# Optimization experiments

Hardware: AMD Instinct MI355X
Metric: run time of the kernel (lower is better)

The kernel has to match this reference:

```python
import jax, jax.numpy as jnp
import numpy as np

BS, IN_F, OUT_F = 1024, 128, 100000
M, S, ALPHA = 0.35, 30.0, 0.5


def _l2norm(x):
    # F.normalize: x / max(||x||, eps)
    n = jnp.sqrt(jnp.sum(x * x, axis=-1, keepdims=True))
    return x / jnp.maximum(n, 1e-12)


def setup_inputs() -> dict:
    key = jax.random.key(0)
    k1, k2, k3 = jax.random.split(key, 3)
    return {
        "input": jax.random.normal(k1, (BS, IN_F), dtype=jnp.float32),
        "label": jax.random.randint(k2, (BS,), 0, OUT_F, dtype=jnp.int64),
        "weight": jax.random.normal(k3, (OUT_F, IN_F), dtype=jnp.float32),
    }


def reference(input, label, weight):
    wn = _l2norm(weight)                      # [nc, d]
    fn = _l2norm(input)                       # [bs, d]
    logits = jnp.einsum('bd,cd->bc', fn, wn)  # [bs, nc] cosine sims
    bs = fn.shape[0]
    rows = jnp.arange(bs)

    pos = jnp.take_along_axis(logits, label[:, None], axis=1)[:, 0] * S  # [bs]
    # negatives: all classes except the label (replaces masked_select + view)
    neg = (logits * S).at[rows, label].set(-jnp.inf)
    lse_neg = jax.nn.logsumexp(neg, axis=1)   # [bs]

    # loss = mean(log(1 + exp(m + lse_neg - pos)))
    loss = jnp.mean(jax.nn.softplus(M + lse_neg - pos))

    # weight.data update: per-class mean of normalized features for classes
    # present in the batch (the torch loop is exactly a segment-mean; note
    # weight_update aliases weight.data so the final blend is a no-op and the
    # result is simply: present rows <- class mean, other rows unchanged).
    sums = jax.ops.segment_sum(fn, label, num_segments=OUT_F)                # [nc, d]
    counts = jax.ops.segment_sum(jnp.ones((bs,), fn.dtype), label, num_segments=OUT_F)
    present = counts > 0
    class_mean = sums / jnp.maximum(counts, 1.0)[:, None]
    new_weight = jnp.where(present[:, None], class_mean, weight)

    return loss, new_weight
```

## Files before the change

kernel.cpp:

```cpp
#include <hip/hip_runtime.h>

#define BS 1024
#define D 128
#define NC 100000
#define NCP 100096
#define NT64 1564
#define PHASES 256
#define S_SCALE 30.0f
#define MARGIN 0.35f
#define S2LOG2E 43.2808512f

typedef __attribute__((ext_vector_type(8))) short bf16x8;
typedef __attribute__((ext_vector_type(4))) float f32x4;

__device__ __forceinline__ unsigned short f2bf(float f) {
    union { float f; unsigned u; } x; x.f = f;
    unsigned u = x.u;
    u += 0x7FFFu + ((u >> 16) & 1u);
    return (unsigned short)(u >> 16);
}

__device__ __forceinline__ void gld_lds16(const void* g, void* l) {
    auto gp = (const __attribute__((address_space(1))) unsigned int*)(g);
    auto lp = (__attribute__((address_space(3))) unsigned int*)(l);
    __builtin_amdgcn_global_load_lds(gp, lp, 16, 0, 0);
}


__global__ void prep_fn(const float* __restrict__ inp, const int* __restrict__ label,
                        const float* __restrict__ wt,
                        float* __restrict__ fn_f32, unsigned short* __restrict__ fn_fr,
                        float* __restrict__ counts, float* __restrict__ pos) {
    int row = blockIdx.x * 4 + (threadIdx.x >> 6);
    int lane = threadIdx.x & 63;
    float2 v = *(const float2*)(inp + row * D + lane * 2);
    float s = v.x * v.x + v.y * v.y;
    #pragma unroll
    for (int m = 1; m < 64; m <<= 1) s += __shfl_xor(s, m);
    float inv = 1.0f / fmaxf(sqrtf(s), 1e-12f);
    float a = v.x * inv, b = v.y * inv;
    *(float2*)(fn_f32 + row * D + lane * 2) = make_float2(a, b);
    unsigned pack = (unsigned)f2bf(a) | ((unsigned)f2bf(b) << 16);
    ((unsigned*)fn_fr)[(row >> 4) * 1024 + (lane >> 2) * 64 + ((row & 15) << 2) + (lane & 3)] = pack;

    int c = label[row];
    float2 wv = *(const float2*)(wt + c * D + lane * 2);
    float sw_ = wv.x * wv.x + wv.y * wv.y;
    float dt  = wv.x * a + wv.y * b;
    #pragma unroll
    for (int m = 1; m < 64; m <<= 1) { sw_ += __shfl_xor(sw_, m); dt += __shfl_xor(dt, m); }
    if (lane == 0) {
        float invw = 1.0f / fmaxf(sqrtf(sw_), 1e-12f);
        pos[row] = S_SCALE * dt * invw;
        atomicAdd(counts + c, 1.0f);
    }
}

__global__ void prep_wn(const float* __restrict__ wt, const float* __restrict__ counts,
                        unsigned short* __restrict__ wn_fr, float* __restrict__ outw) {
    int wv = threadIdx.x >> 6, lane = threadIdx.x & 63;
    int row = blockIdx.x * 4 + wv;
    unsigned* dst = (unsigned*)wn_fr + (row >> 4) * 1024 + (lane >> 2) * 64 +
                    ((row & 15) << 2) + (lane & 3);
    if (row < NC) {
        float2 v = *(const float2*)(wt + row * D + lane * 2);
        float s = v.x * v.x + v.y * v.y;
        #pragma unroll
        for (int m = 1; m < 64; m <<= 1) s += __shfl_xor(s, m);
        float inv = 1.0f / fmaxf(sqrtf(s), 1e-12f);
        *dst = (unsigned)f2bf(v.x * inv) | ((unsigned)f2bf(v.y * inv) << 16);
        float cnt = counts[row];
        float2 o = (cnt > 0.0f) ? make_float2(0.0f, 0.0f) : v;
        *(float2*)(outw + row * D + lane * 2) = o;
    } else {
        *dst = 0u;
    }
}

__global__ __launch_bounds__(1024, 4) void main_gemm(
    const unsigned short* __restrict__ fnfr, const unsigned short* __restrict__ wnfr,
    float* __restrict__ sumexp) {
    __shared__ __align__(16) short Ws[2][8192];
    int tid = threadIdx.x;
    int lane = tid & 63, w = tid >> 6;
    int half = blockIdx.y;
    int rb0 = half * 32 + w * 2;

    bf16x8 bf[2][4];
    {
        const char* gB = (const char*)fnfr + (size_t)rb0 * 4096 + lane * 16;
        #pragma unroll
        for (int cg = 0; cg < 2; cg++)
            #pragma unroll
            for (int ks = 0; ks < 4; ks++)
                bf[cg][ks] = *(const bf16x8*)(gB + cg * 4096 + ks * 1024);
    }
    #pragma unroll
    for (int cg = 0; cg < 2; cg++)
        #pragma unroll
        for (int ks = 0; ks < 4; ks++)
            asm volatile("" : "+v"(bf[cg][ks]));

    float sums[2] = {0.0f, 0.0f};

    int t0 = blockIdx.x;
    {
        const char* g = (const char*)wnfr + (size_t)t0 * 16384 + w * 1024 + lane * 16;
        gld_lds16(g, (char*)Ws[0] + w * 1024);
    }
    __syncthreads();

    int cur = 0;
    for (int t = t0; t < NT64; t += PHASES) {
        int nxt = t + PHASES;
        if (nxt < NT64) {
            const char* g = (const char*)wnfr + (size_t)nxt * 16384 + w * 1024 + lane * 16;
            gld_lds16(g, (char*)Ws[cur ^ 1] + w * 1024);
        }

        f32x4 acc[4][2];
        #pragma unroll
        for (int ag = 0; ag < 4; ag++)
            #pragma unroll
            for (int cg = 0; cg < 2; cg++)
                acc[ag][cg] = (f32x4){0.0f, 0.0f, 0.0f, 0.0f};

        const char* W = (const char*)Ws[cur];
        #pragma unroll
        for (int ks = 0; ks < 4; ks++) {
            bf16x8 a[4];
            #pragma unroll
            for (int ag = 0; ag < 4; ag++)
                a[ag] = *(const bf16x8*)(W + ag * 4096 + ks * 1024 + lane * 16);
            #pragma unroll
            for (int ag = 0; ag < 4; ag++)
                #pragma unroll
                for (int cg = 0; cg < 2; cg++)
                    acc[ag][cg] = __builtin_amdgcn_mfma_f32_16x16x32_bf16(
                        a[ag], bf[cg][ks], acc[ag][cg], 0, 0, 0);
        }

        #pragma unroll
        for (int ag = 0; ag < 4; ag++)
            #pragma unroll
            for (int cg = 0; cg < 2; cg++)
                #pragma unroll
                for (int r = 0; r < 4; r++)
                    sums[cg] += __builtin_amdgcn_exp2f(
                        fmaf(acc[ag][cg][r], S2LOG2E, -S2LOG2E));

        __syncthreads();
        cur ^= 1;
    }

    #pragma unroll
    for (int cg = 0; cg < 2; cg++) {
        float s = sums[cg];
        s += __shfl_xor(s, 16);
        s += __shfl_xor(s, 32);
        if (lane < 16)
            atomicAdd(sumexp + half * 512 + w * 32 + cg * 16 + lane, s);
    }
}

__global__ void loss_k(const float* __restrict__ sumexp, const float* __restrict__ pos,
                       float* __restrict__ out) {
    __shared__ float red[256];
    int t = threadIdx.x;
    float acc = 0.0f;
    #pragma unroll
    for (int i = 0; i < 4; i++) {
        int r = t + i * 256;
        float p = pos[r];
        float sneg = fmaxf(sumexp[r] - __expf(p - 30.0f), 1e-38f);
        float lse = 30.0f + logf(sneg);
        float z = MARGIN + lse - p;
        acc += fmaxf(z, 0.0f) + log1pf(__expf(-fabsf(z)));
    }
    red[t] = acc;
    __syncthreads();
    for (int s = 128; s > 0; s >>= 1) {
        if (t < s) red[t] += red[t + s];
        __syncthreads();
    }
    if (t == 0) out[0] = red[0] * (1.0f / 1024.0f);
}

__global__ void addmean_k(const float* __restrict__ fn_f32, const int* __restrict__ label,
                          const float* __restrict__ counts, float* __restrict__ outw) {
    int b = blockIdx.x, t = threadIdx.x;
    int c = label[b];
    float cnt = counts[c];
    atomicAdd(outw + c * D + t, fn_f32[b * D + t] / cnt);
}

extern "C" void kernel_launch(void* const* d_in, const int* in_sizes, int n_in,
                              void* d_out, int out_size, void* d_ws, size_t ws_size,
                              hipStream_t stream) {
    (void)in_sizes; (void)n_in; (void)out_size; (void)ws_size;
    const float* inp   = (const float*)d_in[0];
    const int*   label = (const int*)d_in[1];
    const float* wt    = (const float*)d_in[2];
    float* out = (float*)d_out;

    char* w = (char*)d_ws;
    float*          fn_f32 = (float*)(w);
    unsigned short* fn_fr  = (unsigned short*)(w + 524288);
    unsigned short* wn_fr  = (unsigned short*)(w + 786432);
    float*          sumexp = (float*)(w + 26411008);
    float*          counts = (float*)(w + 26415104);
    float*          pos    = (float*)(w + 26815104);

    hipMemsetAsync(w + 26411008, 0, 404096, stream);

    prep_fn<<<BS / 4, 256, 0, stream>>>(inp, label, wt, fn_f32, fn_fr, counts, pos);
    prep_wn<<<NCP / 4, 256, 0, stream>>>(wt, counts, wn_fr, out + 1);
    main_gemm<<<dim3(PHASES, 2), 1024, 0, stream>>>(fn_fr, wn_fr, sumexp);
    addmean_k<<<BS, D, 0, stream>>>(fn_f32, label, counts, out + 1);
    loss_k<<<1, 256, 0, stream>>>(sumexp, pos, out);
}
```

Measured before the change: 160.3 us.

## Fuse weight normalization into GEMM and merge tail kernels

Removes the separate prep_wn pass by having the GEMM load fp32 weight rows directly, normalize and convert them to bf16 in registers, and write them into the LDS double buffer. The half-0 blocks also write the untouched weight rows to the output. The addmean and loss kernels are merged into one launch. This drops a 25MB bf16 intermediate write and read plus two launches. In exchange, each of the two y-halves now reads the fp32 weights (twice the bytes of bf16) and adds normalization ALU work inside the GEMM loop.

```diff
diff --git a/kernel.cpp b/kernel.cpp
--- a/kernel.cpp
+++ b/kernel.cpp
@@ -20,12 +20,6 @@
     return (unsigned short)(u >> 16);
 }
 
-__device__ __forceinline__ void gld_lds16(const void* g, void* l) {
-    auto gp = (const __attribute__((address_space(1))) unsigned int*)(g);
-    auto lp = (__attribute__((address_space(3))) unsigned int*)(l);
-    __builtin_amdgcn_global_load_lds(gp, lp, 16, 0, 0);
-}
-
 
 __global__ void prep_fn(const float* __restrict__ inp, const int* __restrict__ label,
                         const float* __restrict__ wt,
@@ -56,39 +50,52 @@
     }
 }
 
-__global__ void prep_wn(const float* __restrict__ wt, const float* __restrict__ counts,
-                        unsigned short* __restrict__ wn_fr, float* __restrict__ outw) {
-    int wv = threadIdx.x >> 6, lane = threadIdx.x & 63;
-    int row = blockIdx.x * 4 + wv;
-    unsigned* dst = (unsigned*)wn_fr + (row >> 4) * 1024 + (lane >> 2) * 64 +
-                    ((row & 15) << 2) + (lane & 3);
-    if (row < NC) {
-        float2 v = *(const float2*)(wt + row * D + lane * 2);
-        float s = v.x * v.x + v.y * v.y;
-        #pragma unroll
-        for (int m = 1; m < 64; m <<= 1) s += __shfl_xor(s, m);
-        float inv = 1.0f / fmaxf(sqrtf(s), 1e-12f);
-        *dst = (unsigned)f2bf(v.x * inv) | ((unsigned)f2bf(v.y * inv) << 16);
-        float cnt = counts[row];
-        float2 o = (cnt > 0.0f) ? make_float2(0.0f, 0.0f) : v;
-        *(float2*)(outw + row * D + lane * 2) = o;
-    } else {
-        *dst = 0u;
-    }
-}
+#define LOADV()  do {                                                         \
+    if (rg < NC) {                                                            \
+        const float* p_ = wt + (size_t)rg * 128 + 2 * g16;                    \
+        v0 = *(const float2*)(p_);      v1 = *(const float2*)(p_ + 32);       \
+        v2 = *(const float2*)(p_ + 64); v3 = *(const float2*)(p_ + 96);       \
+    } else { v0 = v1 = v2 = v3 = make_float2(0.f, 0.f); }                     \
+} while (0)
+
+#define COMMIT(buf) do {                                                      \
+    float ss = v0.x*v0.x + v0.y*v0.y + v1.x*v1.x + v1.y*v1.y                  \
+             + v2.x*v2.x + v2.y*v2.y + v3.x*v3.x + v3.y*v3.y;                 \
+    ss += __shfl_xor(ss, 1); ss += __shfl_xor(ss, 2);                         \
+    ss += __shfl_xor(ss, 4); ss += __shfl_xor(ss, 8);                         \
+    float inv = 1.0f / fmaxf(sqrtf(ss), 1e-12f);                              \
+    unsigned* Wu_ = (unsigned*)(buf);                                         \
+    int base_ = (rloc >> 4) * 1024 + (g16 >> 2) * 64 + (rloc & 15) * 4 + (g16 & 3); \
+    Wu_[base_]       = (unsigned)f2bf(v0.x*inv) | ((unsigned)f2bf(v0.y*inv) << 16); \
+    Wu_[base_ + 256] = (unsigned)f2bf(v1.x*inv) | ((unsigned)f2bf(v1.y*inv) << 16); \
+    Wu_[base_ + 512] = (unsigned)f2bf(v2.x*inv) | ((unsigned)f2bf(v2.y*inv) << 16); \
+    Wu_[base_ + 768] = (unsigned)f2bf(v3.x*inv) | ((unsigned)f2bf(v3.y*inv) << 16); \
+    if (writeout && rg < NC) {                                                \
+        float cnt_ = counts[rg];                                              \
+        float* op_ = outw + (size_t)rg * 128 + 2 * g16;                       \
+        float2 z_ = make_float2(0.f, 0.f);                                    \
+        *(float2*)(op_)      = (cnt_ > 0.f) ? z_ : v0;                        \
+        *(float2*)(op_ + 32) = (cnt_ > 0.f) ? z_ : v1;                        \
+        *(float2*)(op_ + 64) = (cnt_ > 0.f) ? z_ : v2;                        \
+        *(float2*)(op_ + 96) = (cnt_ > 0.f) ? z_ : v3;                        \
+    }                                                                         \
+} while (0)
 
 __global__ __launch_bounds__(1024, 4) void main_gemm(
-    const unsigned short* __restrict__ fnfr, const unsigned short* __restrict__ wnfr,
-    float* __restrict__ sumexp) {
+    const unsigned short* __restrict__ fnfr, const float* __restrict__ wt,
+    const float* __restrict__ counts, float* __restrict__ sumexp,
+    float* __restrict__ outw) {
     __shared__ __align__(16) short Ws[2][8192];
-    int tid = threadIdx.x;
-    int lane = tid & 63, w = tid >> 6;
-    int half = blockIdx.y;
-    int rb0 = half * 32 + w * 2;
+    const int tid = threadIdx.x;
+    const int lane = tid & 63, w = tid >> 6;
+    const int g16 = tid & 15;
+    const int rloc = tid >> 4;
+    const int half = blockIdx.y;
+    const bool writeout = (half == 0);
 
     bf16x8 bf[2][4];
     {
-        const char* gB = (const char*)fnfr + (size_t)rb0 * 4096 + lane * 16;
+        const char* gB = (const char*)fnfr + (size_t)(half * 32 + w * 2) * 4096 + lane * 16;
         #pragma unroll
         for (int cg = 0; cg < 2; cg++)
             #pragma unroll
@@ -102,21 +109,17 @@
             asm volatile("" : "+v"(bf[cg][ks]));
 
     float sums[2] = {0.0f, 0.0f};
-
-    int t0 = blockIdx.x;
-    {
-        const char* g = (const char*)wnfr + (size_t)t0 * 16384 + w * 1024 + lane * 16;
-        gld_lds16(g, (char*)Ws[0] + w * 1024);
-    }
+    float2 v0, v1, v2, v3;
+
+    int rg = blockIdx.x * 64 + rloc;
+    LOADV();
+    COMMIT(Ws[0]);
     __syncthreads();
 
     int cur = 0;
-    for (int t = t0; t < NT64; t += PHASES) {
+    for (int t = blockIdx.x; t < NT64; t += PHASES) {
         int nxt = t + PHASES;
-        if (nxt < NT64) {
-            const char* g = (const char*)wnfr + (size_t)nxt * 16384 + w * 1024 + lane * 16;
-            gld_lds16(g, (char*)Ws[cur ^ 1] + w * 1024);
-        }
+        if (nxt < NT64) { rg = nxt * 64 + rloc; LOADV(); }
 
         f32x4 acc[4][2];
         #pragma unroll
@@ -128,27 +131,29 @@
         const char* W = (const char*)Ws[cur];
         #pragma unroll
         for (int ks = 0; ks < 4; ks++) {
-            bf16x8 a[4];
-            #pragma unroll
-            for (int ag = 0; ag < 4; ag++)
-                a[ag] = *(const bf16x8*)(W + ag * 4096 + ks * 1024 + lane * 16);
-            #pragma unroll
-            for (int ag = 0; ag < 4; ag++)
-                #pragma unroll
-                for (int cg = 0; cg < 2; cg++)
-                    acc[ag][cg] = __builtin_amdgcn_mfma_f32_16x16x32_bf16(
-                        a[ag], bf[cg][ks], acc[ag][cg], 0, 0, 0);
+            bf16x8 a0 = *(const bf16x8*)(W +     0 + ks * 1024 + lane * 16);
+            bf16x8 a1 = *(const bf16x8*)(W +  4096 + ks * 1024 + lane * 16);
+            bf16x8 a2 = *(const bf16x8*)(W +  8192 + ks * 1024 + lane * 16);
+            bf16x8 a3 = *(const bf16x8*)(W + 12288 + ks * 1024 + lane * 16);
+            acc[0][0] = __builtin_amdgcn_mfma_f32_16x16x32_bf16(a0, bf[0][ks], acc[0][0], 0, 0, 0);
+            acc[0][1] = __builtin_amdgcn_mfma_f32_16x16x32_bf16(a0, bf[1][ks], acc[0][1], 0, 0, 0);
+            acc[1][0] = __builtin_amdgcn_mfma_f32_16x16x32_bf16(a1, bf[0][ks], acc[1][0], 0, 0, 0);
+            acc[1][1] = __builtin_amdgcn_mfma_f32_16x16x32_bf16(a1, bf[1][ks], acc[1][1], 0, 0, 0);
+            acc[2][0] = __builtin_amdgcn_mfma_f32_16x16x32_bf16(a2, bf[0][ks], acc[2][0], 0, 0, 0);
+            acc[2][1] = __builtin_amdgcn_mfma_f32_16x16x32_bf16(a2, bf[1][ks], acc[2][1], 0, 0, 0);
+            acc[3][0] = __builtin_amdgcn_mfma_f32_16x16x32_bf16(a3, bf[0][ks], acc[3][0], 0, 0, 0);
+            acc[3][1] = __builtin_amdgcn_mfma_f32_16x16x32_bf16(a3, bf[1][ks], acc[3][1], 0, 0, 0);
         }
 
         #pragma unroll
         for (int ag = 0; ag < 4; ag++)
             #pragma unroll
-            for (int cg = 0; cg < 2; cg++)
-                #pragma unroll
-                for (int r = 0; r < 4; r++)
-                    sums[cg] += __builtin_amdgcn_exp2f(
-                        fmaf(acc[ag][cg][r], S2LOG2E, -S2LOG2E));
-
+            for (int r = 0; r < 4; r++) {
+                sums[0] += __builtin_amdgcn_exp2f(fmaf(acc[ag][0][r], S2LOG2E, -S2LOG2E));
+                sums[1] += __builtin_amdgcn_exp2f(fmaf(acc[ag][1][r], S2LOG2E, -S2LOG2E));
+            }
+
+        if (nxt < NT64) COMMIT(Ws[cur ^ 1]);
         __syncthreads();
         cur ^= 1;
     }
@@ -163,8 +168,17 @@
     }
 }
 
-__global__ void loss_k(const float* __restrict__ sumexp, const float* __restrict__ pos,
+__global__ void tail_k(const float* __restrict__ fn_f32, const int* __restrict__ label,
+                       const float* __restrict__ counts, float* __restrict__ outw,
+                       const float* __restrict__ sumexp, const float* __restrict__ pos,
                        float* __restrict__ out) {
+    if (blockIdx.x < 512) {
+        int b = blockIdx.x * 2 + (threadIdx.x >> 7);
+        int t = threadIdx.x & 127;
+        int c = label[b];
+        atomicAdd(outw + (size_t)c * D + t, fn_f32[b * D + t] / counts[c]);
+        return;
+    }
     __shared__ float red[256];
     int t = threadIdx.x;
     float acc = 0.0f;
@@ -184,14 +198,6 @@
         __syncthreads();
     }
     if (t == 0) out[0] = red[0] * (1.0f / 1024.0f);
-}
-
-__global__ void addmean_k(const float* __restrict__ fn_f32, const int* __restrict__ label,
-                          const float* __restrict__ counts, float* __restrict__ outw) {
-    int b = blockIdx.x, t = threadIdx.x;
-    int c = label[b];
-    float cnt = counts[c];
-    atomicAdd(outw + c * D + t, fn_f32[b * D + t] / cnt);
 }
 
 extern "C" void kernel_launch(void* const* d_in, const int* in_sizes, int n_in,
@@ -206,7 +212,6 @@
     char* w = (char*)d_ws;
     float*          fn_f32 = (float*)(w);
     unsigned short* fn_fr  = (unsigned short*)(w + 524288);
-    unsigned short* wn_fr  = (unsigned short*)(w + 786432);
     float*          sumexp = (float*)(w + 26411008);
     float*          counts = (float*)(w + 26415104);
     float*          pos    = (float*)(w + 26815104);
@@ -214,8 +219,6 @@
     hipMemsetAsync(w + 26411008, 0, 404096, stream);
 
     prep_fn<<<BS / 4, 256, 0, stream>>>(inp, label, wt, fn_f32, fn_fr, counts, pos);
-    prep_wn<<<NCP / 4, 256, 0, stream>>>(wt, counts, wn_fr, out + 1);
-    main_gemm<<<dim3(PHASES, 2), 1024, 0, stream>>>(fn_fr, wn_fr, sumexp);
-    addmean_k<<<BS, D, 0, stream>>>(fn_f32, label, counts, out + 1);
-    loss_k<<<1, 256, 0, stream>>>(sumexp, pos, out);
-}
+    main_gemm<<<dim3(PHASES, 2), 1024, 0, stream>>>(fn_fr, wt, counts, sumexp, out + 1);
+    tail_k<<<513, 256, 0, stream>>>(fn_f32, label, counts, out + 1, sumexp, pos, out);
+}
```

Measured after the change: 139.3 us. 13.1% less time.
